# Performance work log

Hardware: AMD Instinct MI355X
Metric: run time of the kernel (lower is better)

## Reference

```python
import jax, jax.numpy as jnp
import numpy as np

N_ATOMS = 100000
N_BONDS = 200000
MAX_NB = 6
N_ATOM_FEATS = 39
N_BOND_FEATS = 11
HIDDEN = 128
DEPTH = 6


def setup_inputs() -> dict:
    key = jax.random.key(0)
    k = jax.random.split(key, 8)
    fatoms = jax.random.normal(k[0], (N_ATOMS, N_ATOM_FEATS), dtype=jnp.float32)
    fbonds = jax.random.normal(k[1], (N_BONDS, N_ATOM_FEATS + N_BOND_FEATS), dtype=jnp.float32)
    agraph = jax.random.randint(k[2], (N_ATOMS, MAX_NB), 0, N_BONDS, dtype=jnp.int32)
    bgraph = jax.random.randint(k[3], (N_BONDS, MAX_NB), 0, N_BONDS, dtype=jnp.int32)
    s_i = 1.0 / np.sqrt(N_ATOM_FEATS + N_BOND_FEATS)
    s_h = 1.0 / np.sqrt(HIDDEN)
    s_o = 1.0 / np.sqrt(N_ATOM_FEATS + HIDDEN)
    W_i = jax.random.uniform(k[4], (HIDDEN, N_ATOM_FEATS + N_BOND_FEATS), jnp.float32, -s_i, s_i)
    W_h = jax.random.uniform(k[5], (HIDDEN, HIDDEN), jnp.float32, -s_h, s_h)
    W_o = jax.random.uniform(k[6], (HIDDEN, N_ATOM_FEATS + HIDDEN), jnp.float32, -s_o, s_o)
    b_o = jax.random.uniform(k[7], (HIDDEN,), jnp.float32, -s_o, s_o)
    return {"fatoms": fatoms, "fbonds": fbonds, "agraph": agraph, "bgraph": bgraph,
            "W_i": W_i, "W_h": W_h, "W_o": W_o, "b_o": b_o}


def reference(fatoms, fbonds, agraph, bgraph, W_i, W_h, W_o, b_o):
    # Input message per directed bond: [n_bonds, hidden]
    binput = fbonds @ W_i.T
    message = jax.nn.relu(binput)
    # Message passing: gather neighbor bond messages, sum, linear, residual-add input, ReLU
    for _ in range(DEPTH - 1):
        nei = jnp.take(message, bgraph, axis=0).sum(axis=1)   # [n_bonds, hidden]
        message = jax.nn.relu(binput + nei @ W_h.T)
    # Aggregate incoming bond messages per atom
    a_nei = jnp.take(message, agraph, axis=0).sum(axis=1)      # [n_atoms, hidden]
    atom_input = jnp.concatenate([fatoms, a_nei], axis=1)      # dropout is identity at eval
    atom_h = jax.nn.relu(atom_input @ W_o.T + b_o)
    return atom_h
```

## Files before the change

kernel.cpp:

```cpp
#include <hip/hip_runtime.h>

#define N_ATOMS   100000
#define N_BONDS   200000
#define MAX_NB    6
#define AF        39
#define BFEAT     50
#define H         128
#define DEPTH     6
#define KS_I      2
#define KS_H      4
#define KS_O      6

typedef unsigned short ushort_t;
typedef unsigned int   uint_t;

typedef __attribute__((ext_vector_type(8))) short  bf16x8;
typedef __attribute__((ext_vector_type(4))) float  f32x4;

__device__ inline float bf2f(ushort_t u) {
    union { uint_t i; float f; } v; v.i = ((uint_t)u) << 16; return v.f;
}
__device__ inline ushort_t f2bf(float f) {
    union { float f; uint_t i; } v; v.f = f;
    uint_t x = v.i;
    uint_t r = (x + 0x7fffu + ((x >> 16) & 1u)) >> 16;
    return (ushort_t)r;
}
__device__ inline uint_t pack2(float a, float b) {
    return (uint_t)f2bf(a) | ((uint_t)f2bf(b) << 16);
}
__device__ inline uint_t relu2(uint_t w) {
    uint_t lo = w & 0xffffu, hi = w >> 16;
    if (lo & 0x8000u) lo = 0;
    if (hi & 0x8000u) hi = 0;
    return lo | (hi << 16);
}
__device__ inline void addv(float* a, uint4 v) {
    a[0] += bf2f((ushort_t)(v.x & 0xffffu)); a[1] += bf2f((ushort_t)(v.x >> 16));
    a[2] += bf2f((ushort_t)(v.y & 0xffffu)); a[3] += bf2f((ushort_t)(v.y >> 16));
    a[4] += bf2f((ushort_t)(v.z & 0xffffu)); a[5] += bf2f((ushort_t)(v.z >> 16));
    a[6] += bf2f((ushort_t)(v.w & 0xffffu)); a[7] += bf2f((ushort_t)(v.w >> 16));
}
__device__ inline void addvr(float* a, uint4 v) {
    v.x = relu2(v.x); v.y = relu2(v.y); v.z = relu2(v.z); v.w = relu2(v.w);
    addv(a, v);
}

__global__ __launch_bounds__(256) void k_pack(const float* __restrict__ W_i,
                                              const float* __restrict__ W_h,
                                              const float* __restrict__ W_o,
                                              ushort_t* __restrict__ pWi,
                                              ushort_t* __restrict__ pWh,
                                              ushort_t* __restrict__ pWo) {
    int id = blockIdx.x * 256 + threadIdx.x;
    int mat;
    ushort_t* dst;
    if (id < 1024)        { mat = 0; dst = pWi; }
    else if (id < 3072)   { mat = 1; dst = pWh; id -= 1024; }
    else                  { mat = 2; dst = pWo; id -= 3072; }
    const int lane = id & 63;
    const int nt   = (id >> 6) & 7;
    const int ks   = id >> 9;
    const int n  = nt * 16 + (lane & 15);
    const int k0 = ks * 32 + (lane >> 4) * 8;
    float v[8];
#pragma unroll
    for (int j = 0; j < 8; ++j) {
        const int k = k0 + j;
        float x = 0.f;
        if (mat == 0)      { if (k < BFEAT) x = W_i[n * BFEAT + k]; }
        else if (mat == 1) { x = W_h[n * H + k]; }
        else {
            if (k < H)          x = W_o[(size_t)n * (AF + H) + AF + k];
            else if (k < H + AF) x = W_o[(size_t)n * (AF + H) + (k - H)];
        }
        v[j] = x;
    }
    uint4 u;
    u.x = pack2(v[0], v[1]); u.y = pack2(v[2], v[3]);
    u.z = pack2(v[4], v[5]); u.w = pack2(v[6], v[7]);
    ((uint4*)dst)[id] = u;
}

__global__ __launch_bounds__(256) void k_binput(const float* __restrict__ fbonds,
                                                const ushort_t* __restrict__ pWi,
                                                ushort_t* __restrict__ binput) {
    __shared__ __align__(16) ushort_t sAC[64][136];
    const int t = threadIdx.x;
    const int b0 = blockIdx.x * 64;

    for (int i = t; i < 64 * 25; i += 256) {
        const int row = i / 25, j = i % 25;
        const float2 v = *(const float2*)(fbonds + (size_t)(b0 + row) * BFEAT + j * 2);
        *(uint_t*)&sAC[row][j * 2] = pack2(v.x, v.y);
    }
    for (int i = t; i < 64 * 7; i += 256) {
        const int row = i / 7, c = BFEAT + (i % 7) * 2;
        *(uint_t*)&sAC[row][c] = 0u;
    }
    __syncthreads();

    const int w    = t >> 6;
    const int lane = t & 63;
    const int col  = lane & 15;
    const int kg   = lane >> 4;
    const int m    = 16 * w + col;

    f32x4 acc[8];
#pragma unroll
    for (int nt = 0; nt < 8; ++nt) acc[nt] = (f32x4){0.f, 0.f, 0.f, 0.f};
    bf16x8 af[KS_I];
#pragma unroll
    for (int ks = 0; ks < KS_I; ++ks)
        af[ks] = *(const bf16x8*)&sAC[m][ks * 32 + kg * 8];
#pragma unroll
    for (int ks = 0; ks < KS_I; ++ks) {
#pragma unroll
        for (int nt = 0; nt < 8; ++nt) {
            const bf16x8 b = *(const bf16x8*)(pWi + (((size_t)(ks * 8 + nt) * 64 + lane) * 8));
            acc[nt] = __builtin_amdgcn_mfma_f32_16x16x32_bf16(af[ks], b, acc[nt], 0, 0, 0);
        }
    }
    const int row0 = kg * 4;
#pragma unroll
    for (int nt = 0; nt < 8; ++nt)
#pragma unroll
        for (int r = 0; r < 4; ++r)
            sAC[16 * w + row0 + r][nt * 16 + col] = f2bf(acc[nt][r]);
    __syncthreads();

    for (int i = t; i < 64 * 16; i += 256) {
        const int row = i >> 4, c0 = (i & 15) * 8;
        const uint4 v = *(const uint4*)&sAC[row][c0];
        *(uint4*)(binput + (size_t)(b0 + row) * H + c0) = v;
    }
}

__global__ __launch_bounds__(256) void k_mp(const ushort_t* __restrict__ msg_in,
                                            const int* __restrict__ bgraph,
                                            const ushort_t* __restrict__ pWh,
                                            const ushort_t* __restrict__ binput,
                                            ushort_t* __restrict__ msg_out) {
    __shared__ __align__(16) ushort_t sAC[64][136];
    __shared__ int sIdx[64][MAX_NB];
    const int t = threadIdx.x;
    const int b0 = blockIdx.x * 64;

    for (int i = t; i < 64 * MAX_NB; i += 256)
        sIdx[i / MAX_NB][i % MAX_NB] = bgraph[(size_t)b0 * MAX_NB + i];
    __syncthreads();

    {
        const int bi = t >> 4;
        const int c0 = (t & 15) * 8;
#pragma unroll
        for (int p = 0; p < 4; p += 2) {
            const int iA = p * 16 + bi;
            const int iB = iA + 16;
            uint4 vA[MAX_NB], vB[MAX_NB];
#pragma unroll
            for (int j = 0; j < MAX_NB; ++j)
                vA[j] = *(const uint4*)(msg_in + (size_t)sIdx[iA][j] * H + c0);
#pragma unroll
            for (int j = 0; j < MAX_NB; ++j)
                vB[j] = *(const uint4*)(msg_in + (size_t)sIdx[iB][j] * H + c0);
            float a[8], b[8];
#pragma unroll
            for (int q = 0; q < 8; ++q) { a[q] = 0.f; b[q] = 0.f; }
#pragma unroll
            for (int j = 0; j < MAX_NB; ++j) addvr(a, vA[j]);
#pragma unroll
            for (int j = 0; j < MAX_NB; ++j) addvr(b, vB[j]);
            uint4 ua, ub;
            ua.x = pack2(a[0], a[1]); ua.y = pack2(a[2], a[3]);
            ua.z = pack2(a[4], a[5]); ua.w = pack2(a[6], a[7]);
            ub.x = pack2(b[0], b[1]); ub.y = pack2(b[2], b[3]);
            ub.z = pack2(b[4], b[5]); ub.w = pack2(b[6], b[7]);
            *(uint4*)&sAC[iA][c0] = ua;
            *(uint4*)&sAC[iB][c0] = ub;
        }
    }
    __syncthreads();

    uint4 biPF[4];
#pragma unroll
    for (int p = 0; p < 4; ++p) {
        const int i = t + p * 256;
        const int row = i >> 4, c0 = (i & 15) * 8;
        biPF[p] = *(const uint4*)(binput + (size_t)(b0 + row) * H + c0);
    }

    const int w    = t >> 6;
    const int lane = t & 63;
    const int col  = lane & 15;
    const int kg   = lane >> 4;
    const int m    = 16 * w + col;

    f32x4 acc[8];
#pragma unroll
    for (int nt = 0; nt < 8; ++nt) acc[nt] = (f32x4){0.f, 0.f, 0.f, 0.f};
    bf16x8 af[KS_H];
#pragma unroll
    for (int ks = 0; ks < KS_H; ++ks)
        af[ks] = *(const bf16x8*)&sAC[m][ks * 32 + kg * 8];
#pragma unroll
    for (int ks = 0; ks < KS_H; ++ks) {
#pragma unroll
        for (int nt = 0; nt < 8; ++nt) {
            const bf16x8 b = *(const bf16x8*)(pWh + (((size_t)(ks * 8 + nt) * 64 + lane) * 8));
            acc[nt] = __builtin_amdgcn_mfma_f32_16x16x32_bf16(af[ks], b, acc[nt], 0, 0, 0);
        }
    }
    const int row0 = kg * 4;
#pragma unroll
    for (int nt = 0; nt < 8; ++nt)
#pragma unroll
        for (int r = 0; r < 4; ++r)
            sAC[16 * w + row0 + r][nt * 16 + col] = f2bf(acc[nt][r]);
    __syncthreads();

#pragma unroll
    for (int p = 0; p < 4; ++p) {
        const int i = t + p * 256;
        const int row = i >> 4, c0 = (i & 15) * 8;
        const size_t off = (size_t)(b0 + row) * H + c0;
        const uint4 bi4 = biPF[p];
        const uint4 cc  = *(const uint4*)&sAC[row][c0];
        uint4 o; float v0, v1;
        v0 = bf2f((ushort_t)(bi4.x & 0xffffu)) + bf2f((ushort_t)(cc.x & 0xffffu));
        v1 = bf2f((ushort_t)(bi4.x >> 16))     + bf2f((ushort_t)(cc.x >> 16));
        o.x = pack2(v0, v1);
        v0 = bf2f((ushort_t)(bi4.y & 0xffffu)) + bf2f((ushort_t)(cc.y & 0xffffu));
        v1 = bf2f((ushort_t)(bi4.y >> 16))     + bf2f((ushort_t)(cc.y >> 16));
        o.y = pack2(v0, v1);
        v0 = bf2f((ushort_t)(bi4.z & 0xffffu)) + bf2f((ushort_t)(cc.z & 0xffffu));
        v1 = bf2f((ushort_t)(bi4.z >> 16))     + bf2f((ushort_t)(cc.z >> 16));
        o.z = pack2(v0, v1);
        v0 = bf2f((ushort_t)(bi4.w & 0xffffu)) + bf2f((ushort_t)(cc.w & 0xffffu));
        v1 = bf2f((ushort_t)(bi4.w >> 16))     + bf2f((ushort_t)(cc.w >> 16));
        o.w = pack2(v0, v1);
        *(uint4*)(msg_out + off) = o;
    }
}

__global__ __launch_bounds__(256) void k_out(const ushort_t* __restrict__ msg,
                                             const int* __restrict__ agraph,
                                             const float* __restrict__ fatoms,
                                             const ushort_t* __restrict__ pWo,
                                             const float* __restrict__ b_o,
                                             float* __restrict__ out) {
    __shared__ __align__(16) unsigned char smem[64 * 132 * 4];
    ushort_t (*sA)[200] = (ushort_t(*)[200])smem;
    float    (*sC)[132] = (float(*)[132])smem;
    __shared__ int sIdx[64][MAX_NB];
    const int t = threadIdx.x;
    const int a0 = blockIdx.x * 64;

    for (int i = t; i < 64 * MAX_NB; i += 256) {
        const int a = a0 + i / MAX_NB;
        sIdx[i / MAX_NB][i % MAX_NB] = (a < N_ATOMS) ? agraph[(size_t)a * MAX_NB + (i % MAX_NB)] : 0;
    }
    for (int i = t; i < 64 * 64; i += 256) {
        const int row = i >> 6, c = i & 63;
        const int a = a0 + row;
        float x = 0.f;
        if (c < AF && a < N_ATOMS) x = fatoms[(size_t)a * AF + c];
        sA[row][H + c] = f2bf(x);
    }
    __syncthreads();

    {
        const int bi = t >> 4;
        const int c0 = (t & 15) * 8;
#pragma unroll
        for (int p = 0; p < 4; p += 2) {
            const int iA = p * 16 + bi;
            const int iB = iA + 16;
            uint4 vA[MAX_NB], vB[MAX_NB];
#pragma unroll
            for (int j = 0; j < MAX_NB; ++j)
                vA[j] = *(const uint4*)(msg + (size_t)sIdx[iA][j] * H + c0);
#pragma unroll
            for (int j = 0; j < MAX_NB; ++j)
                vB[j] = *(const uint4*)(msg + (size_t)sIdx[iB][j] * H + c0);
            float a[8], b[8];
#pragma unroll
            for (int q = 0; q < 8; ++q) { a[q] = 0.f; b[q] = 0.f; }
#pragma unroll
            for (int j = 0; j < MAX_NB; ++j) addvr(a, vA[j]);
#pragma unroll
            for (int j = 0; j < MAX_NB; ++j) addvr(b, vB[j]);
            uint4 ua, ub;
            ua.x = pack2(a[0], a[1]); ua.y = pack2(a[2], a[3]);
            ua.z = pack2(a[4], a[5]); ua.w = pack2(a[6], a[7]);
            ub.x = pack2(b[0], b[1]); ub.y = pack2(b[2], b[3]);
            ub.z = pack2(b[4], b[5]); ub.w = pack2(b[6], b[7]);
            *(uint4*)&sA[iA][c0] = ua;
            *(uint4*)&sA[iB][c0] = ub;
        }
    }
    __syncthreads();

    const int w    = t >> 6;
    const int lane = t & 63;
    const int col  = lane & 15;
    const int kg   = lane >> 4;
    const int m    = 16 * w + col;

    f32x4 acc[8];
#pragma unroll
    for (int nt = 0; nt < 8; ++nt) acc[nt] = (f32x4){0.f, 0.f, 0.f, 0.f};
#pragma unroll
    for (int ks = 0; ks < KS_O; ++ks) {
        const bf16x8 a = *(const bf16x8*)&sA[m][ks * 32 + kg * 8];
#pragma unroll
        for (int nt = 0; nt < 8; ++nt) {
            const bf16x8 b = *(const bf16x8*)(pWo + (((size_t)(ks * 8 + nt) * 64 + lane) * 8));
            acc[nt] = __builtin_amdgcn_mfma_f32_16x16x32_bf16(a, b, acc[nt], 0, 0, 0);
        }
    }
    __syncthreads();

    const int row0 = kg * 4;
#pragma unroll
    for (int nt = 0; nt < 8; ++nt)
#pragma unroll
        for (int r = 0; r < 4; ++r)
            sC[16 * w + row0 + r][nt * 16 + col] = acc[nt][r];
    __syncthreads();

    const float4* bo4 = (const float4*)b_o;
    for (int i = t; i < 64 * 16; i += 256) {
        const int row = i >> 4, c0 = (i & 15) * 8;
        const int a = a0 + row;
        if (a < N_ATOMS) {
            const float* cp = &sC[row][c0];
            const float4 b1 = bo4[c0 >> 2];
            const float4 b2 = bo4[(c0 >> 2) + 1];
            float4 o1, o2;
            o1.x = cp[0] + b1.x; o1.y = cp[1] + b1.y; o1.z = cp[2] + b1.z; o1.w = cp[3] + b1.w;
            o2.x = cp[4] + b2.x; o2.y = cp[5] + b2.y; o2.z = cp[6] + b2.z; o2.w = cp[7] + b2.w;
            o1.x = o1.x > 0.f ? o1.x : 0.f; o1.y = o1.y > 0.f ? o1.y : 0.f;
            o1.z = o1.z > 0.f ? o1.z : 0.f; o1.w = o1.w > 0.f ? o1.w : 0.f;
            o2.x = o2.x > 0.f ? o2.x : 0.f; o2.y = o2.y > 0.f ? o2.y : 0.f;
            o2.z = o2.z > 0.f ? o2.z : 0.f; o2.w = o2.w > 0.f ? o2.w : 0.f;
            float* op = out + (size_t)a * H + c0;
            *(float4*)op = o1;
            *(float4*)(op + 4) = o2;
        }
    }
}

extern "C" void kernel_launch(void* const* d_in, const int* in_sizes, int n_in,
                              void* d_out, int out_size, void* d_ws, size_t ws_size,
                              hipStream_t stream) {
    const float* fatoms = (const float*)d_in[0];
    const float* fbonds = (const float*)d_in[1];
    const int*   agraph = (const int*)d_in[2];
    const int*   bgraph = (const int*)d_in[3];
    const float* W_i    = (const float*)d_in[4];
    const float* W_h    = (const float*)d_in[5];
    const float* W_o    = (const float*)d_in[6];
    const float* b_o    = (const float*)d_in[7];
    float* out = (float*)d_out;

    const size_t MSG_BYTES = (size_t)N_BONDS * H * sizeof(ushort_t);
    char* ws = (char*)d_ws;
    ushort_t* binput = (ushort_t*)(ws);
    ushort_t* msgA   = (ushort_t*)(ws + MSG_BYTES);
    ushort_t* msgB   = (ushort_t*)(ws + 2 * MSG_BYTES);
    ushort_t* pWi    = (ushort_t*)(ws + 3 * MSG_BYTES);
    ushort_t* pWh    = (ushort_t*)(ws + 3 * MSG_BYTES + 16 * 1024);
    ushort_t* pWo    = (ushort_t*)(ws + 3 * MSG_BYTES + 48 * 1024);

    k_pack<<<24, 256, 0, stream>>>(W_i, W_h, W_o, pWi, pWh, pWo);
    k_binput<<<N_BONDS / 64, 256, 0, stream>>>(fbonds, pWi, binput);

    ushort_t* bufs[2] = { msgA, msgB };
    const ushort_t* cur = binput;
    for (int d = 0; d < DEPTH - 1; ++d) {
        ushort_t* nxt = bufs[d & 1];
        k_mp<<<N_BONDS / 64, 256, 0, stream>>>(cur, bgraph, pWh, binput, nxt);
        cur = nxt;
    }

    k_out<<<(N_ATOMS + 63) / 64, 256, 0, stream>>>(cur, agraph, fatoms, pWo, b_o, out);
}
```

Before: 517.7 us.

## Recompute binput inside message-passing GEMM via concatenated W_i|W_h weights

Each message-passing step now recomputes the bond input projection inside its GEMM. It concatenates the bf16 bond features (64 wide) with the neighbor sum and multiplies by a packed [W_i | W_h] weight. This removes the 256B/row binput read and the separate add epilogue, and it stores post-ReLU messages so the gather no longer needs ReLU masking. It also switches to the hardware v_cvt_pk_bf16_f32 conversion and a cheaper bf16 unpack. The cost is 50% more MFMA work per step and a slightly different rounding path.

```diff
diff --git a/kernel.cpp b/kernel.cpp
--- a/kernel.cpp
+++ b/kernel.cpp
@@ -8,8 +8,9 @@
 #define H         128
 #define DEPTH     6
 #define KS_I      2
-#define KS_H      4
+#define KS_IH     6
 #define KS_O      6
+#define FBW       64
 
 typedef unsigned short ushort_t;
 typedef unsigned int   uint_t;
@@ -17,47 +18,37 @@
 typedef __attribute__((ext_vector_type(8))) short  bf16x8;
 typedef __attribute__((ext_vector_type(4))) float  f32x4;
 
-__device__ inline float bf2f(ushort_t u) {
-    union { uint_t i; float f; } v; v.i = ((uint_t)u) << 16; return v.f;
-}
-__device__ inline ushort_t f2bf(float f) {
-    union { float f; uint_t i; } v; v.f = f;
-    uint_t x = v.i;
-    uint_t r = (x + 0x7fffu + ((x >> 16) & 1u)) >> 16;
-    return (ushort_t)r;
-}
-__device__ inline uint_t pack2(float a, float b) {
-    return (uint_t)f2bf(a) | ((uint_t)f2bf(b) << 16);
-}
-__device__ inline uint_t relu2(uint_t w) {
-    uint_t lo = w & 0xffffu, hi = w >> 16;
-    if (lo & 0x8000u) lo = 0;
-    if (hi & 0x8000u) hi = 0;
-    return lo | (hi << 16);
-}
+__device__ inline uint_t cvt_pk(float lo, float hi) {
+    uint_t r;
+    asm("v_cvt_pk_bf16_f32 %0, %1, %2" : "=v"(r) : "v"(lo), "v"(hi));
+    return r;
+}
+__device__ inline ushort_t f2bf(float f) { return (ushort_t)cvt_pk(f, f); }
+
 __device__ inline void addv(float* a, uint4 v) {
-    a[0] += bf2f((ushort_t)(v.x & 0xffffu)); a[1] += bf2f((ushort_t)(v.x >> 16));
-    a[2] += bf2f((ushort_t)(v.y & 0xffffu)); a[3] += bf2f((ushort_t)(v.y >> 16));
-    a[4] += bf2f((ushort_t)(v.z & 0xffffu)); a[5] += bf2f((ushort_t)(v.z >> 16));
-    a[6] += bf2f((ushort_t)(v.w & 0xffffu)); a[7] += bf2f((ushort_t)(v.w >> 16));
-}
-__device__ inline void addvr(float* a, uint4 v) {
-    v.x = relu2(v.x); v.y = relu2(v.y); v.z = relu2(v.z); v.w = relu2(v.w);
-    addv(a, v);
+    union { uint_t u; float f; } c;
+    c.u = v.x << 16;          a[0] += c.f;
+    c.u = v.x & 0xffff0000u;  a[1] += c.f;
+    c.u = v.y << 16;          a[2] += c.f;
+    c.u = v.y & 0xffff0000u;  a[3] += c.f;
+    c.u = v.z << 16;          a[4] += c.f;
+    c.u = v.z & 0xffff0000u;  a[5] += c.f;
+    c.u = v.w << 16;          a[6] += c.f;
+    c.u = v.w & 0xffff0000u;  a[7] += c.f;
 }
 
 __global__ __launch_bounds__(256) void k_pack(const float* __restrict__ W_i,
                                               const float* __restrict__ W_h,
                                               const float* __restrict__ W_o,
                                               ushort_t* __restrict__ pWi,
-                                              ushort_t* __restrict__ pWh,
+                                              ushort_t* __restrict__ pWih,
                                               ushort_t* __restrict__ pWo) {
     int id = blockIdx.x * 256 + threadIdx.x;
     int mat;
     ushort_t* dst;
-    if (id < 1024)        { mat = 0; dst = pWi; }
-    else if (id < 3072)   { mat = 1; dst = pWh; id -= 1024; }
-    else                  { mat = 2; dst = pWo; id -= 3072; }
+    if (id < 1024)      { mat = 0; dst = pWi; }
+    else if (id < 4096) { mat = 1; dst = pWih; id -= 1024; }
+    else                { mat = 2; dst = pWo;  id -= 4096; }
     const int lane = id & 63;
     const int nt   = (id >> 6) & 7;
     const int ks   = id >> 9;
@@ -68,23 +59,27 @@
     for (int j = 0; j < 8; ++j) {
         const int k = k0 + j;
         float x = 0.f;
-        if (mat == 0)      { if (k < BFEAT) x = W_i[n * BFEAT + k]; }
-        else if (mat == 1) { x = W_h[n * H + k]; }
-        else {
-            if (k < H)          x = W_o[(size_t)n * (AF + H) + AF + k];
+        if (mat == 0) {
+            if (k < BFEAT) x = W_i[n * BFEAT + k];
+        } else if (mat == 1) {
+            if (k < BFEAT)     x = W_i[n * BFEAT + k];
+            else if (k >= FBW) x = W_h[n * H + (k - FBW)];
+        } else {
+            if (k < H)           x = W_o[(size_t)n * (AF + H) + AF + k];
             else if (k < H + AF) x = W_o[(size_t)n * (AF + H) + (k - H)];
         }
         v[j] = x;
     }
     uint4 u;
-    u.x = pack2(v[0], v[1]); u.y = pack2(v[2], v[3]);
-    u.z = pack2(v[4], v[5]); u.w = pack2(v[6], v[7]);
+    u.x = cvt_pk(v[0], v[1]); u.y = cvt_pk(v[2], v[3]);
+    u.z = cvt_pk(v[4], v[5]); u.w = cvt_pk(v[6], v[7]);
     ((uint4*)dst)[id] = u;
 }
 
 __global__ __launch_bounds__(256) void k_binput(const float* __restrict__ fbonds,
                                                 const ushort_t* __restrict__ pWi,
-                                                ushort_t* __restrict__ binput) {
+                                                ushort_t* __restrict__ fbb,
+                                                ushort_t* __restrict__ msg0) {
     __shared__ __align__(16) ushort_t sAC[64][136];
     const int t = threadIdx.x;
     const int b0 = blockIdx.x * 64;
@@ -92,13 +87,18 @@
     for (int i = t; i < 64 * 25; i += 256) {
         const int row = i / 25, j = i % 25;
         const float2 v = *(const float2*)(fbonds + (size_t)(b0 + row) * BFEAT + j * 2);
-        *(uint_t*)&sAC[row][j * 2] = pack2(v.x, v.y);
+        *(uint_t*)&sAC[row][j * 2] = cvt_pk(v.x, v.y);
     }
     for (int i = t; i < 64 * 7; i += 256) {
         const int row = i / 7, c = BFEAT + (i % 7) * 2;
         *(uint_t*)&sAC[row][c] = 0u;
     }
     __syncthreads();
+
+    for (int i = t; i < 64 * 8; i += 256) {
+        const int row = i >> 3, c0 = (i & 7) * 8;
+        *(uint4*)(fbb + (size_t)(b0 + row) * FBW + c0) = *(const uint4*)&sAC[row][c0];
+    }
 
     const int w    = t >> 6;
     const int lane = t & 63;
@@ -121,31 +121,36 @@
             acc[nt] = __builtin_amdgcn_mfma_f32_16x16x32_bf16(af[ks], b, acc[nt], 0, 0, 0);
         }
     }
+    __syncthreads();
+
     const int row0 = kg * 4;
 #pragma unroll
     for (int nt = 0; nt < 8; ++nt)
 #pragma unroll
         for (int r = 0; r < 4; ++r)
-            sAC[16 * w + row0 + r][nt * 16 + col] = f2bf(acc[nt][r]);
+            sAC[16 * w + row0 + r][nt * 16 + col] = f2bf(fmaxf(acc[nt][r], 0.f));
     __syncthreads();
 
     for (int i = t; i < 64 * 16; i += 256) {
         const int row = i >> 4, c0 = (i & 15) * 8;
-        const uint4 v = *(const uint4*)&sAC[row][c0];
-        *(uint4*)(binput + (size_t)(b0 + row) * H + c0) = v;
+        *(uint4*)(msg0 + (size_t)(b0 + row) * H + c0) = *(const uint4*)&sAC[row][c0];
     }
 }
 
 __global__ __launch_bounds__(256) void k_mp(const ushort_t* __restrict__ msg_in,
                                             const int* __restrict__ bgraph,
-                                            const ushort_t* __restrict__ pWh,
-                                            const ushort_t* __restrict__ binput,
+                                            const ushort_t* __restrict__ pWih,
+                                            const ushort_t* __restrict__ fbb,
                                             ushort_t* __restrict__ msg_out) {
-    __shared__ __align__(16) ushort_t sAC[64][136];
+    __shared__ __align__(16) ushort_t sAC[64][200];
     __shared__ int sIdx[64][MAX_NB];
     const int t = threadIdx.x;
     const int b0 = blockIdx.x * 64;
 
+    for (int i = t; i < 64 * 8; i += 256) {
+        const int row = i >> 3, c0 = (i & 7) * 8;
+        *(uint4*)&sAC[row][c0] = *(const uint4*)(fbb + (size_t)(b0 + row) * FBW + c0);
+    }
     for (int i = t; i < 64 * MAX_NB; i += 256)
         sIdx[i / MAX_NB][i % MAX_NB] = bgraph[(size_t)b0 * MAX_NB + i];
     __syncthreads();
@@ -168,27 +173,19 @@
 #pragma unroll
             for (int q = 0; q < 8; ++q) { a[q] = 0.f; b[q] = 0.f; }
 #pragma unroll
-            for (int j = 0; j < MAX_NB; ++j) addvr(a, vA[j]);
-#pragma unroll
-            for (int j = 0; j < MAX_NB; ++j) addvr(b, vB[j]);
+            for (int j = 0; j < MAX_NB; ++j) addv(a, vA[j]);
+#pragma unroll
+            for (int j = 0; j < MAX_NB; ++j) addv(b, vB[j]);
             uint4 ua, ub;
-            ua.x = pack2(a[0], a[1]); ua.y = pack2(a[2], a[3]);
-            ua.z = pack2(a[4], a[5]); ua.w = pack2(a[6], a[7]);
-            ub.x = pack2(b[0], b[1]); ub.y = pack2(b[2], b[3]);
-            ub.z = pack2(b[4], b[5]); ub.w = pack2(b[6], b[7]);
-            *(uint4*)&sAC[iA][c0] = ua;
-            *(uint4*)&sAC[iB][c0] = ub;
-        }
-    }
-    __syncthreads();
-
-    uint4 biPF[4];
-#pragma unroll
-    for (int p = 0; p < 4; ++p) {
-        const int i = t + p * 256;
-        const int row = i >> 4, c0 = (i & 15) * 8;
-        biPF[p] = *(const uint4*)(binput + (size_t)(b0 + row) * H + c0);
-    }
+            ua.x = cvt_pk(a[0], a[1]); ua.y = cvt_pk(a[2], a[3]);
+            ua.z = cvt_pk(a[4], a[5]); ua.w = cvt_pk(a[6], a[7]);
+            ub.x = cvt_pk(b[0], b[1]); ub.y = cvt_pk(b[2], b[3]);
+            ub.z = cvt_pk(b[4], b[5]); ub.w = cvt_pk(b[6], b[7]);
+            *(uint4*)&sAC[iA][FBW + c0] = ua;
+            *(uint4*)&sAC[iB][FBW + c0] = ub;
+        }
+    }
+    __syncthreads();
 
     const int w    = t >> 6;
     const int lane = t & 63;
@@ -199,15 +196,15 @@
     f32x4 acc[8];
 #pragma unroll
     for (int nt = 0; nt < 8; ++nt) acc[nt] = (f32x4){0.f, 0.f, 0.f, 0.f};
-    bf16x8 af[KS_H];
-#pragma unroll
-    for (int ks = 0; ks < KS_H; ++ks)
+    bf16x8 af[KS_IH];
+#pragma unroll
+    for (int ks = 0; ks < KS_IH; ++ks)
         af[ks] = *(const bf16x8*)&sAC[m][ks * 32 + kg * 8];
 #pragma unroll
-    for (int ks = 0; ks < KS_H; ++ks) {
+    for (int ks = 0; ks < KS_IH; ++ks) {
 #pragma unroll
         for (int nt = 0; nt < 8; ++nt) {
-            const bf16x8 b = *(const bf16x8*)(pWh + (((size_t)(ks * 8 + nt) * 64 + lane) * 8));
+            const bf16x8 b = *(const bf16x8*)(pWih + (((size_t)(ks * 8 + nt) * 64 + lane) * 8));
             acc[nt] = __builtin_amdgcn_mfma_f32_16x16x32_bf16(af[ks], b, acc[nt], 0, 0, 0);
         }
     }
@@ -216,30 +213,12 @@
     for (int nt = 0; nt < 8; ++nt)
 #pragma unroll
         for (int r = 0; r < 4; ++r)
-            sAC[16 * w + row0 + r][nt * 16 + col] = f2bf(acc[nt][r]);
-    __syncthreads();
-
-#pragma unroll
-    for (int p = 0; p < 4; ++p) {
-        const int i = t + p * 256;
+            sAC[16 * w + row0 + r][nt * 16 + col] = f2bf(fmaxf(acc[nt][r], 0.f));
+    __syncthreads();
+
+    for (int i = t; i < 64 * 16; i += 256) {
         const int row = i >> 4, c0 = (i & 15) * 8;
-        const size_t off = (size_t)(b0 + row) * H + c0;
-        const uint4 bi4 = biPF[p];
-        const uint4 cc  = *(const uint4*)&sAC[row][c0];
-        uint4 o; float v0, v1;
-        v0 = bf2f((ushort_t)(bi4.x & 0xffffu)) + bf2f((ushort_t)(cc.x & 0xffffu));
-        v1 = bf2f((ushort_t)(bi4.x >> 16))     + bf2f((ushort_t)(cc.x >> 16));
-        o.x = pack2(v0, v1);
-        v0 = bf2f((ushort_t)(bi4.y & 0xffffu)) + bf2f((ushort_t)(cc.y & 0xffffu));
-        v1 = bf2f((ushort_t)(bi4.y >> 16))     + bf2f((ushort_t)(cc.y >> 16));
-        o.y = pack2(v0, v1);
-        v0 = bf2f((ushort_t)(bi4.z & 0xffffu)) + bf2f((ushort_t)(cc.z & 0xffffu));
-        v1 = bf2f((ushort_t)(bi4.z >> 16))     + bf2f((ushort_t)(cc.z >> 16));
-        o.z = pack2(v0, v1);
-        v0 = bf2f((ushort_t)(bi4.w & 0xffffu)) + bf2f((ushort_t)(cc.w & 0xffffu));
-        v1 = bf2f((ushort_t)(bi4.w >> 16))     + bf2f((ushort_t)(cc.w >> 16));
-        o.w = pack2(v0, v1);
-        *(uint4*)(msg_out + off) = o;
+        *(uint4*)(msg_out + (size_t)(b0 + row) * H + c0) = *(const uint4*)&sAC[row][c0];
     }
 }
 
@@ -287,14 +266,14 @@
 #pragma unroll
             for (int q = 0; q < 8; ++q) { a[q] = 0.f; b[q] = 0.f; }
 #pragma unroll
-            for (int j = 0; j < MAX_NB; ++j) addvr(a, vA[j]);
-#pragma unroll
-            for (int j = 0; j < MAX_NB; ++j) addvr(b, vB[j]);
+            for (int j = 0; j < MAX_NB; ++j) addv(a, vA[j]);
+#pragma unroll
+            for (int j = 0; j < MAX_NB; ++j) addv(b, vB[j]);
             uint4 ua, ub;
-            ua.x = pack2(a[0], a[1]); ua.y = pack2(a[2], a[3]);
-            ua.z = pack2(a[4], a[5]); ua.w = pack2(a[6], a[7]);
-            ub.x = pack2(b[0], b[1]); ub.y = pack2(b[2], b[3]);
-            ub.z = pack2(b[4], b[5]); ub.w = pack2(b[6], b[7]);
+            ua.x = cvt_pk(a[0], a[1]); ua.y = cvt_pk(a[2], a[3]);
+            ua.z = cvt_pk(a[4], a[5]); ua.w = cvt_pk(a[6], a[7]);
+            ub.x = cvt_pk(b[0], b[1]); ub.y = cvt_pk(b[2], b[3]);
+            ub.z = cvt_pk(b[4], b[5]); ub.w = cvt_pk(b[6], b[7]);
             *(uint4*)&sA[iA][c0] = ua;
             *(uint4*)&sA[iB][c0] = ub;
         }
@@ -365,23 +344,23 @@
     float* out = (float*)d_out;
 
     const size_t MSG_BYTES = (size_t)N_BONDS * H * sizeof(ushort_t);
+    const size_t FBB_BYTES = (size_t)N_BONDS * FBW * sizeof(ushort_t);
     char* ws = (char*)d_ws;
-    ushort_t* binput = (ushort_t*)(ws);
-    ushort_t* msgA   = (ushort_t*)(ws + MSG_BYTES);
-    ushort_t* msgB   = (ushort_t*)(ws + 2 * MSG_BYTES);
-    ushort_t* pWi    = (ushort_t*)(ws + 3 * MSG_BYTES);
-    ushort_t* pWh    = (ushort_t*)(ws + 3 * MSG_BYTES + 16 * 1024);
-    ushort_t* pWo    = (ushort_t*)(ws + 3 * MSG_BYTES + 48 * 1024);
-
-    k_pack<<<24, 256, 0, stream>>>(W_i, W_h, W_o, pWi, pWh, pWo);
-    k_binput<<<N_BONDS / 64, 256, 0, stream>>>(fbonds, pWi, binput);
-
-    ushort_t* bufs[2] = { msgA, msgB };
-    const ushort_t* cur = binput;
+    ushort_t* m0   = (ushort_t*)(ws);
+    ushort_t* m1   = (ushort_t*)(ws + MSG_BYTES);
+    ushort_t* fbb  = (ushort_t*)(ws + 2 * MSG_BYTES);
+    ushort_t* pWi  = (ushort_t*)(ws + 2 * MSG_BYTES + FBB_BYTES);
+    ushort_t* pWih = (ushort_t*)(ws + 2 * MSG_BYTES + FBB_BYTES + 16 * 1024);
+    ushort_t* pWo  = (ushort_t*)(ws + 2 * MSG_BYTES + FBB_BYTES + 64 * 1024);
+
+    k_pack<<<28, 256, 0, stream>>>(W_i, W_h, W_o, pWi, pWih, pWo);
+    k_binput<<<N_BONDS / 64, 256, 0, stream>>>(fbonds, pWi, fbb, m0);
+
+    ushort_t* cur = m0;
+    ushort_t* nxt = m1;
     for (int d = 0; d < DEPTH - 1; ++d) {
-        ushort_t* nxt = bufs[d & 1];
-        k_mp<<<N_BONDS / 64, 256, 0, stream>>>(cur, bgraph, pWh, binput, nxt);
-        cur = nxt;
+        k_mp<<<N_BONDS / 64, 256, 0, stream>>>(cur, bgraph, pWih, fbb, nxt);
+        ushort_t* tmp = cur; cur = nxt; nxt = tmp;
     }
 
     k_out<<<(N_ATOMS + 63) / 64, 256, 0, stream>>>(cur, agraph, fatoms, pWo, b_o, out);
```

After: 475.9 us. -8.1%, faster.
